# Kernel optimization log

Hardware: AMD Instinct MI355X
Metric: run time of the kernel (lower is better)

The kernel has to match this reference:

```python
import jax, jax.numpy as jnp
import numpy as np

EMB = 768
HEADS = 8
HEAD_DIM = EMB // HEADS  # 96
SCALING = HEAD_DIM ** -0.5


def setup_inputs() -> dict:
    key = jax.random.key(0)
    ks = jax.random.split(key, 9)
    B, S = 2, 2048
    std = 1.0 / np.sqrt(EMB)
    x = jax.random.normal(ks[0], (B, S, EMB), dtype=jnp.float32)
    # torch nn.Linear weights are [out, in]; we store [in, out] for x @ W.
    Wq = jax.random.normal(ks[1], (EMB, EMB), dtype=jnp.float32) * std
    Wk = jax.random.normal(ks[2], (EMB, EMB), dtype=jnp.float32) * std
    Wv = jax.random.normal(ks[3], (EMB, EMB), dtype=jnp.float32) * std
    Wo = jax.random.normal(ks[4], (EMB, EMB), dtype=jnp.float32) * std
    bq = jax.random.normal(ks[5], (EMB,), dtype=jnp.float32) * std
    bk = jax.random.normal(ks[6], (EMB,), dtype=jnp.float32) * std
    bv = jax.random.normal(ks[7], (EMB,), dtype=jnp.float32) * std
    bo = jax.random.normal(ks[8], (EMB,), dtype=jnp.float32) * std
    return {"x": x, "Wq": Wq, "bq": bq, "Wk": Wk, "bk": bk,
            "Wv": Wv, "bv": bv, "Wo": Wo, "bo": bo}


def _split_heads(t):
    # [B, S, E] -> [B, H, S, D]
    B, S, _ = t.shape
    return t.reshape(B, S, HEADS, HEAD_DIM).transpose(0, 2, 1, 3)


def reference(x, Wq, bq, Wk, bk, Wv, bv, Wo, bo):
    q = _split_heads(x @ Wq + bq)
    k = _split_heads(x @ Wk + bk)
    v = _split_heads(x @ Wv + bv)
    # Full [B, H, S, S] score matrix, as in the source module.
    energies = jnp.einsum('bhqd,bhkd->bhqk', q, k)
    # Faithful quirk: softmax first, THEN multiply by scaling (dropout=0 -> identity).
    attention = jax.nn.softmax(energies, axis=-1) * SCALING
    out = jnp.einsum('bhqk,bhkd->bhqd', attention, v)
    B, H, S, D = out.shape
    out = out.transpose(0, 2, 1, 3).reshape(B, S, H * D)
    return out @ Wo + bo
```

## Files before the change

kernel.cpp:

```cpp
#include <hip/hip_runtime.h>
#include <hip/hip_bf16.h>

#define EMB 768
#define HD 96
#define NH 8
#define SEQ 2048
#define SCALING 0.10206207261596575f

typedef short bf16x8 __attribute__((ext_vector_type(8)));
typedef float f32x4  __attribute__((ext_vector_type(4)));
typedef unsigned short u16v8 __attribute__((ext_vector_type(8)));
typedef unsigned short u16v4 __attribute__((ext_vector_type(4)));

union F4 { float4 v; float f[4]; };

__device__ __forceinline__ unsigned short f2bf(float v) {
    __hip_bfloat16 b = __float2bfloat16(v);
    return *reinterpret_cast<unsigned short*>(&b);
}
__device__ __forceinline__ float bf2f(unsigned short u) {
    __hip_bfloat16 b = *reinterpret_cast<__hip_bfloat16*>(&u);
    return __bfloat162float(b);
}

__device__ __forceinline__ void dma16(const unsigned short* g, unsigned short* l) {
    __builtin_amdgcn_global_load_lds(
        (const __attribute__((address_space(1))) unsigned int*)g,
        (__attribute__((address_space(3))) unsigned int*)l,
        16, 0, 0);
}

__global__ __launch_bounds__(256) void convert_x(
    const float* __restrict__ x,
    unsigned short* __restrict__ xh, unsigned short* __restrict__ xl)
{
    const size_t i0 = ((size_t)blockIdx.x * 256 + threadIdx.x) * 8;
    F4 a, b;
    a.v = *(const float4*)&x[i0];
    b.v = *(const float4*)&x[i0 + 4];
    u16v8 h, l;
    #pragma unroll
    for (int j = 0; j < 4; j++) {
        unsigned short hu = f2bf(a.f[j]);
        h[j] = hu; l[j] = f2bf(a.f[j] - bf2f(hu));
    }
    #pragma unroll
    for (int j = 0; j < 4; j++) {
        unsigned short hu = f2bf(b.f[j]);
        h[4+j] = hu; l[4+j] = f2bf(b.f[j] - bf2f(hu));
    }
    *(u16v8*)&xh[i0] = h;
    *(u16v8*)&xl[i0] = l;
}

__global__ __launch_bounds__(256) void convert_wT(
    const float* __restrict__ Wq, const float* __restrict__ Wk,
    const float* __restrict__ Wv, const float* __restrict__ Wo,
    unsigned short* __restrict__ WhT, unsigned short* __restrict__ WlT)
{
    const int z = blockIdx.z;
    const float* W = (z == 0) ? Wq : (z == 1) ? Wk : (z == 2) ? Wv : Wo;
    unsigned short* oh = WhT + (size_t)z * 589824;
    unsigned short* ol = WlT + (size_t)z * 589824;
    __shared__ float T[64][68];
    const int t = threadIdx.x;
    const int r = t >> 2, cg = (t & 3) * 16;
    const int k0 = blockIdx.x * 64, n0 = blockIdx.y * 64;
    #pragma unroll
    for (int i = 0; i < 4; i++) {
        float4 v = *(const float4*)&W[(size_t)(k0 + r) * EMB + n0 + cg + 4*i];
        *(float4*)&T[r][cg + 4*i] = v;
    }
    __syncthreads();
    #pragma unroll
    for (int i = 0; i < 4; i++) {
        u16v4 h, l;
        #pragma unroll
        for (int j = 0; j < 4; j++) {
            float v = T[cg + 4*i + j][r];
            unsigned short hu = f2bf(v);
            h[j] = hu; l[j] = f2bf(v - bf2f(hu));
        }
        *(u16v4*)&oh[(size_t)(n0 + r) * EMB + k0 + cg + 4*i] = h;
        *(u16v4*)&ol[(size_t)(n0 + r) * EMB + k0 + cg + 4*i] = l;
    }
}

#define QA_H 0
#define QA_L 4096
#define QW_H 8192
#define QW_L 12288

__global__ __launch_bounds__(256, 3) void qkv_mfma(
    const unsigned short* __restrict__ xh, const unsigned short* __restrict__ xl,
    const unsigned short* __restrict__ WhT, const unsigned short* __restrict__ WlT,
    const float* __restrict__ bq, const float* __restrict__ bk, const float* __restrict__ bv,
    unsigned short* __restrict__ Qh, unsigned short* __restrict__ Ql,
    unsigned short* __restrict__ Kb, unsigned short* __restrict__ Vt)
{
    const int which = blockIdx.z;
    const unsigned short* Wh = WhT + (size_t)which * 589824;
    const unsigned short* Wl = WlT + (size_t)which * 589824;
    const float* bias = (which == 0) ? bq : (which == 1) ? bk : bv;

    __shared__ __align__(16) unsigned short lds[16384];
    const int tid = threadIdx.x;
    const int lane = tid & 63, lo = lane & 15, h4 = lane >> 4;
    const int w = tid >> 6, wm = w & 1, wn = w >> 1;
    const int row0 = blockIdx.x * 128, col0 = blockIdx.y * 128;

    const unsigned short* sbase =
        (w == 0) ? xh + (size_t)row0 * EMB :
        (w == 1) ? xl + (size_t)row0 * EMB :
        (w == 2) ? Wh + (size_t)col0 * EMB :
                   Wl + (size_t)col0 * EMB;
    const int soff = w * 4096;

    f32x4 acc[4][4];
    #pragma unroll
    for (int i = 0; i < 4; i++)
        #pragma unroll
        for (int j = 0; j < 4; j++) acc[i][j] = (f32x4){0.f, 0.f, 0.f, 0.f};

    for (int k0 = 0; k0 < EMB; k0 += 32) {
        #pragma unroll
        for (int j = 0; j < 8; j++) {
            const int u = j*64 + lane;
            const int row = u >> 2, c8 = (u & 3) * 8;
            dma16(sbase + (size_t)row * EMB + k0 + c8, &lds[soff + j*512]);
        }
        __syncthreads();

        bf16x8 ah[4], al[4];
        #pragma unroll
        for (int i = 0; i < 4; i++)
            ah[i] = *(const bf16x8*)&lds[QA_H + (64*wm + 16*i + lo)*32 + 8*h4];
        if (which <= 1) {
            #pragma unroll
            for (int i = 0; i < 4; i++)
                al[i] = *(const bf16x8*)&lds[QA_L + (64*wm + 16*i + lo)*32 + 8*h4];
        }
        #pragma unroll
        for (int j = 0; j < 4; j++) {
            bf16x8 whf = *(const bf16x8*)&lds[QW_H + (64*wn + 16*j + lo)*32 + 8*h4];
            #pragma unroll
            for (int i = 0; i < 4; i++)
                acc[i][j] = __builtin_amdgcn_mfma_f32_16x16x32_bf16(ah[i], whf, acc[i][j], 0, 0, 0);
            if (which <= 1) {
                #pragma unroll
                for (int i = 0; i < 4; i++)
                    acc[i][j] = __builtin_amdgcn_mfma_f32_16x16x32_bf16(al[i], whf, acc[i][j], 0, 0, 0);
            }
            if (which != 1) {
                bf16x8 wlf = *(const bf16x8*)&lds[QW_L + (64*wn + 16*j + lo)*32 + 8*h4];
                #pragma unroll
                for (int i = 0; i < 4; i++)
                    acc[i][j] = __builtin_amdgcn_mfma_f32_16x16x32_bf16(ah[i], wlf, acc[i][j], 0, 0, 0);
            }
        }
        __syncthreads();
    }

    if (which == 0) {
        #pragma unroll
        for (int i = 0; i < 4; i++)
            #pragma unroll
            for (int r = 0; r < 4; r++) {
                const int sg = row0 + 64*wm + 16*i + 4*h4 + r;
                const int b = sg >> 11, s = sg & 2047;
                #pragma unroll
                for (int j = 0; j < 4; j++) {
                    const int c = col0 + 64*wn + 16*j + lo;
                    const int h = c / HD, d = c - h*HD;
                    float v = acc[i][j][r] + bias[c];
                    unsigned short hu = f2bf(v);
                    const size_t base = ((size_t)(b*NH + h) * SEQ + s) * HD + d;
                    Qh[base] = hu;
                    Ql[base] = f2bf(v - bf2f(hu));
                }
            }
    } else if (which == 1) {
        #pragma unroll
        for (int i = 0; i < 4; i++)
            #pragma unroll
            for (int r = 0; r < 4; r++) {
                const int sg = row0 + 64*wm + 16*i + 4*h4 + r;
                const int b = sg >> 11, s = sg & 2047;
                #pragma unroll
                for (int j = 0; j < 4; j++) {
                    const int c = col0 + 64*wn + 16*j + lo;
                    const int h = c / HD, d = c - h*HD;
                    float v = acc[i][j][r] + bias[c];
                    Kb[((size_t)(b*NH + h) * SEQ + s) * HD + d] = f2bf(v);
                }
            }
    } else {
        #pragma unroll
        for (int i = 0; i < 4; i++)
            #pragma unroll
            for (int r = 0; r < 4; r++) {
                const int sg = row0 + 64*wm + 16*i + 4*h4 + r;
                const int b = sg >> 11, s = sg & 2047;
                #pragma unroll
                for (int j = 0; j < 4; j++) {
                    const int c = col0 + 64*wn + 16*j + lo;
                    const int h = c / HD, d = c - h*HD;
                    float v = acc[i][j][r] + bias[c];
                    Vt[((size_t)(b*NH + h) * HD + d) * SEQ + s] = f2bf(v);
                }
            }
    }
}

#define PA_O 0
#define PWH_O 4096
#define PWL_O 6144

__global__ __launch_bounds__(256, 3) void proj_mfma(
    const unsigned short* __restrict__ AOh,
    const unsigned short* __restrict__ Wh, const unsigned short* __restrict__ Wl,
    const float* __restrict__ bo, float* __restrict__ out)
{
    __shared__ __align__(16) unsigned short lds[8192];
    const int tid = threadIdx.x;
    const int lane = tid & 63, lo = lane & 15, h4 = lane >> 4;
    const int w = tid >> 6, wm = w & 1, wn = w >> 1;
    const int row0 = blockIdx.x * 128, col0 = blockIdx.y * 64;

    const unsigned short* sbase =
        (w <= 1) ? AOh + (size_t)row0 * EMB :
        (w == 2) ? Wh  + (size_t)col0 * EMB :
                   Wl  + (size_t)col0 * EMB;
    const int jbase = (w == 1) ? 4 : 0;
    const int soff  = (w <= 1) ? PA_O : (w == 2) ? PWH_O : PWL_O;

    f32x4 acc[4][2];
    #pragma unroll
    for (int i = 0; i < 4; i++)
        #pragma unroll
        for (int j = 0; j < 2; j++) acc[i][j] = (f32x4){0.f, 0.f, 0.f, 0.f};

    for (int k0 = 0; k0 < EMB; k0 += 32) {
        #pragma unroll
        for (int jj = 0; jj < 4; jj++) {
            const int j = jbase + jj;
            const int u = j*64 + lane;
            const int row = u >> 2, c8 = (u & 3) * 8;
            dma16(sbase + (size_t)row * EMB + k0 + c8, &lds[soff + j*512]);
        }
        __syncthreads();

        bf16x8 af[4];
        #pragma unroll
        for (int i = 0; i < 4; i++)
            af[i] = *(const bf16x8*)&lds[PA_O + (64*wm + 16*i + lo)*32 + 8*h4];
        #pragma unroll
        for (int j = 0; j < 2; j++) {
            bf16x8 whf = *(const bf16x8*)&lds[PWH_O + (32*wn + 16*j + lo)*32 + 8*h4];
            bf16x8 wlf = *(const bf16x8*)&lds[PWL_O + (32*wn + 16*j + lo)*32 + 8*h4];
            #pragma unroll
            for (int i = 0; i < 4; i++) {
                acc[i][j] = __builtin_amdgcn_mfma_f32_16x16x32_bf16(af[i], whf, acc[i][j], 0, 0, 0);
                acc[i][j] = __builtin_amdgcn_mfma_f32_16x16x32_bf16(af[i], wlf, acc[i][j], 0, 0, 0);
            }
        }
        __syncthreads();
    }

    #pragma unroll
    for (int i = 0; i < 4; i++)
        #pragma unroll
        for (int r = 0; r < 4; r++) {
            const int sg = row0 + 64*wm + 16*i + 4*h4 + r;
            #pragma unroll
            for (int j = 0; j < 2; j++) {
                const int c = col0 + 32*wn + 16*j + lo;
                out[(size_t)sg * EMB + c] = acc[i][j][r] + bo[c];
            }
        }
}

#define AKB0 0
#define AVB0 6656
#define ABUF 13568
#define AP_OFF 27136

__global__ __launch_bounds__(256, 1) void attn_mfma(
    const unsigned short* __restrict__ Qh, const unsigned short* __restrict__ Ql,
    const unsigned short* __restrict__ Kb, const unsigned short* __restrict__ Vt,
    unsigned short* __restrict__ AOh)
{
    __shared__ __align__(16) unsigned short lds[36352];
    const int id   = blockIdx.x;
    const int xcd  = id & 7;
    const int j    = id >> 3;
    const int bh   = 2*xcd + (j & 1);
    const int q0   = (j >> 1) * 128;
    const int tid  = threadIdx.x;
    const int w    = tid >> 6;
    const int lane = tid & 63;
    const int lo   = lane & 15;
    const int h4   = lane >> 4;

    bf16x8 qhf[2][3], qlf[2][3];
    #pragma unroll
    for (int mi = 0; mi < 2; mi++) {
        const size_t qoff = ((size_t)bh*SEQ + q0 + 32*w + 16*mi + lo) * HD + 8*h4;
        #pragma unroll
        for (int ks = 0; ks < 3; ks++) {
            qhf[mi][ks] = *(const bf16x8*)&Qh[qoff + 32*ks];
            qlf[mi][ks] = *(const bf16x8*)&Ql[qoff + 32*ks];
        }
    }

    f32x4 O[2][6];
    #pragma unroll
    for (int mi = 0; mi < 2; mi++)
        #pragma unroll
        for (int i = 0; i < 6; i++) O[mi][i] = (f32x4){0.f, 0.f, 0.f, 0.f};
    float lsum[2][4] = {};

    unsigned short* Pw = lds + AP_OFF + w * 2304;
    const unsigned short* KbH = Kb + (size_t)bh * SEQ * HD;
    const unsigned short* VtH = Vt + (size_t)bh * HD * SEQ;

    #pragma unroll
    for (int r = 0; r < 3; r++) {
        const int u = tid + 256*r;
        const int kk = u / 12, g = u - kk*12;
        *(u16v8*)&lds[AKB0 + kk*104 + 8*g] = *(const u16v8*)&KbH[kk*HD + 8*g];
        const int dV = u >> 3, c8 = u & 7;
        *(u16v8*)&lds[AVB0 + dV*72 + 8*c8] = *(const u16v8*)&VtH[(size_t)dV*SEQ + 8*c8];
    }
    __syncthreads();

    #pragma unroll 1
    for (int c = 0; c < 32; c++) {
        unsigned short* curK = lds + (c & 1) * ABUF;
        unsigned short* curV = curK + 6656;
        unsigned short* nxtK = lds + ((c + 1) & 1) * ABUF;
        unsigned short* nxtV = nxtK + 6656;
        const int kn = (c + 1 < 32) ? (c + 1) * 64 : 0;

        u16v8 kst[3], vst[3];
        {
            const unsigned short* KG = KbH + (size_t)kn * HD;
            const unsigned short* VG = VtH + kn;
            #pragma unroll
            for (int r = 0; r < 3; r++) {
                const int u = tid + 256*r;
                const int kk = u / 12, g = u - kk*12;
                kst[r] = *(const u16v8*)&KG[kk*HD + 8*g];
                const int dV = u >> 3, c8 = u & 7;
                vst[r] = *(const u16v8*)&VG[(size_t)dV*SEQ + 8*c8];
            }
        }

        f32x4 S[2][4];
        #pragma unroll
        for (int mi = 0; mi < 2; mi++)
            #pragma unroll
            for (int nb = 0; nb < 4; nb++) S[mi][nb] = (f32x4){0.f, 0.f, 0.f, 0.f};
        #pragma unroll
        for (int ks = 0; ks < 3; ks++) {
            bf16x8 kf[4];
            #pragma unroll
            for (int nb = 0; nb < 4; nb++)
                kf[nb] = *(const bf16x8*)&curK[(16*nb + lo)*104 + 32*ks + 8*h4];
            #pragma unroll
            for (int nb = 0; nb < 4; nb++)
                #pragma unroll
                for (int mi = 0; mi < 2; mi++) {
                    S[mi][nb] = __builtin_amdgcn_mfma_f32_16x16x32_bf16(qhf[mi][ks], kf[nb], S[mi][nb], 0, 0, 0);
                    S[mi][nb] = __builtin_amdgcn_mfma_f32_16x16x32_bf16(qlf[mi][ks], kf[nb], S[mi][nb], 0, 0, 0);
                }
        }

        #pragma unroll
        for (int mi = 0; mi < 2; mi++)
            #pragma unroll
            for (int nb = 0; nb < 4; nb++)
                #pragma unroll
                for (int r = 0; r < 4; r++) {
                    float p = __expf(S[mi][nb][r]);
                    lsum[mi][r] += p;
                    Pw[(16*mi + 4*h4 + r)*72 + 16*nb + lo] = f2bf(p);
                }

        #pragma unroll
        for (int ks2 = 0; ks2 < 2; ks2++) {
            bf16x8 pf0 = *(const bf16x8*)&Pw[(lo)*72      + 32*ks2 + 8*h4];
            bf16x8 pf1 = *(const bf16x8*)&Pw[(16 + lo)*72 + 32*ks2 + 8*h4];
            #pragma unroll
            for (int nb2 = 0; nb2 < 6; nb2++) {
                bf16x8 vfv = *(const bf16x8*)&curV[(16*nb2 + lo)*72 + 32*ks2 + 8*h4];
                O[0][nb2] = __builtin_amdgcn_mfma_f32_16x16x32_bf16(pf0, vfv, O[0][nb2], 0, 0, 0);
                O[1][nb2] = __builtin_amdgcn_mfma_f32_16x16x32_bf16(pf1, vfv, O[1][nb2], 0, 0, 0);
            }
        }

        #pragma unroll
        for (int r = 0; r < 3; r++) {
            const int u = tid + 256*r;
            const int kk = u / 12, g = u - kk*12;
            *(u16v8*)&nxtK[kk*104 + 8*g] = kst[r];
            const int dV = u >> 3, c8 = u & 7;
            *(u16v8*)&nxtV[dV*72 + 8*c8] = vst[r];
        }
        __syncthreads();
    }

    const int b = bh >> 3, hh = bh & 7;
    #pragma unroll
    for (int mi = 0; mi < 2; mi++)
        #pragma unroll
        for (int r = 0; r < 4; r++) {
            float l = lsum[mi][r];
            l += __shfl_xor(l, 1);
            l += __shfl_xor(l, 2);
            l += __shfl_xor(l, 4);
            l += __shfl_xor(l, 8);
            const float sc = SCALING / l;
            const int q = q0 + 32*w + 16*mi + 4*h4 + r;
            const size_t base = ((size_t)b*SEQ + q)*EMB + hh*HD + lo;
            #pragma unroll
            for (int nb2 = 0; nb2 < 6; nb2++)
                AOh[base + 16*nb2] = f2bf(O[mi][nb2][r] * sc);
        }
}

extern "C" void kernel_launch(void* const* d_in, const int* in_sizes, int n_in,
                              void* d_out, int out_size, void* d_ws, size_t ws_size,
                              hipStream_t stream)
{
    const float* x  = (const float*)d_in[0];
    const float* Wq = (const float*)d_in[1];
    const float* bq = (const float*)d_in[2];
    const float* Wk = (const float*)d_in[3];
    const float* bk = (const float*)d_in[4];
    const float* Wv = (const float*)d_in[5];
    const float* bv = (const float*)d_in[6];
    const float* Wo = (const float*)d_in[7];
    const float* bo = (const float*)d_in[8];
    float* out = (float*)d_out;

    unsigned short* ws = (unsigned short*)d_ws;
    const size_t HS = (size_t)16 * SEQ * HD;
    const size_t WS1 = (size_t)EMB * EMB;
    unsigned short* Qh  = ws;
    unsigned short* Ql  = ws + HS;
    unsigned short* Kb  = ws + 2*HS;
    unsigned short* Vt  = ws + 3*HS;
    unsigned short* xh  = ws + 4*HS;
    unsigned short* xl  = ws + 5*HS;
    unsigned short* WhT = ws + 6*HS;
    unsigned short* WlT = ws + 6*HS + 4*WS1;
    unsigned short* AOh = xh;

    convert_x<<<1536, 256, 0, stream>>>(x, xh, xl);
    convert_wT<<<dim3(12, 12, 4), 256, 0, stream>>>(Wq, Wk, Wv, Wo, WhT, WlT);
    qkv_mfma<<<dim3(32, 6, 3), 256, 0, stream>>>(xh, xl, WhT, WlT, bq, bk, bv,
                                                 Qh, Ql, Kb, Vt);
    attn_mfma<<<256, 256, 0, stream>>>(Qh, Ql, Kb, Vt, AOh);
    proj_mfma<<<dim3(32, 12), 256, 0, stream>>>(AOh, WhT + 3*WS1, WlT + 3*WS1, bo, out);
}
```

Before: 215.8 us.

## Split attention block into 8 waves of 16 query rows each

The attention kernel now runs 512 threads per block, with each wave owning 16 query rows instead of 32. Per-wave register state (Q fragments, O accumulators, S tiles) is halved, and the K/V tile staging is spread over more threads, so each thread issues one load per round instead of two. The aim is more waves per CU to hide latency. In exchange, each K/V fragment read from LDS now feeds only one query tile, which doubles LDS read traffic per unit of MFMA work, and block-wide barriers now cover 8 waves.

Result: faster. 207.7 us (-3.8%).

```diff
diff --git a/kernel.cpp b/kernel.cpp
--- a/kernel.cpp
+++ b/kernel.cpp
@@ -285,7 +285,7 @@
 #define ABUF 13568
 #define AP_OFF 27136
 
-__global__ __launch_bounds__(256, 1) void attn_mfma(
+__global__ __launch_bounds__(512, 2) void attn_mfma(
     const unsigned short* __restrict__ Qh, const unsigned short* __restrict__ Ql,
     const unsigned short* __restrict__ Kb, const unsigned short* __restrict__ Vt,
     unsigned short* __restrict__ AOh)
@@ -302,35 +302,36 @@
     const int lo   = lane & 15;
     const int h4   = lane >> 4;
 
-    bf16x8 qhf[2][3], qlf[2][3];
-    #pragma unroll
-    for (int mi = 0; mi < 2; mi++) {
-        const size_t qoff = ((size_t)bh*SEQ + q0 + 32*w + 16*mi + lo) * HD + 8*h4;
+    bf16x8 qhf[3], qlf[3];
+    {
+        const size_t qoff = ((size_t)bh*SEQ + q0 + 16*w + lo) * HD + 8*h4;
         #pragma unroll
         for (int ks = 0; ks < 3; ks++) {
-            qhf[mi][ks] = *(const bf16x8*)&Qh[qoff + 32*ks];
-            qlf[mi][ks] = *(const bf16x8*)&Ql[qoff + 32*ks];
-        }
-    }
-
-    f32x4 O[2][6];
-    #pragma unroll
-    for (int mi = 0; mi < 2; mi++)
-        #pragma unroll
-        for (int i = 0; i < 6; i++) O[mi][i] = (f32x4){0.f, 0.f, 0.f, 0.f};
-    float lsum[2][4] = {};
-
-    unsigned short* Pw = lds + AP_OFF + w * 2304;
+            qhf[ks] = *(const bf16x8*)&Qh[qoff + 32*ks];
+            qlf[ks] = *(const bf16x8*)&Ql[qoff + 32*ks];
+        }
+    }
+
+    f32x4 O[6];
+    #pragma unroll
+    for (int i = 0; i < 6; i++) O[i] = (f32x4){0.f, 0.f, 0.f, 0.f};
+    float lsum[4] = {};
+
+    unsigned short* Pw = lds + AP_OFF + w * 1152;
     const unsigned short* KbH = Kb + (size_t)bh * SEQ * HD;
     const unsigned short* VtH = Vt + (size_t)bh * HD * SEQ;
 
     #pragma unroll
     for (int r = 0; r < 3; r++) {
-        const int u = tid + 256*r;
-        const int kk = u / 12, g = u - kk*12;
-        *(u16v8*)&lds[AKB0 + kk*104 + 8*g] = *(const u16v8*)&KbH[kk*HD + 8*g];
-        const int dV = u >> 3, c8 = u & 7;
-        *(u16v8*)&lds[AVB0 + dV*72 + 8*c8] = *(const u16v8*)&VtH[(size_t)dV*SEQ + 8*c8];
+        const int u = tid + 512*r;
+        if (u < 768) {
+            const int kk = u / 12, g = u - kk*12;
+            *(u16v8*)&lds[AKB0 + kk*104 + 8*g] = *(const u16v8*)&KbH[kk*HD + 8*g];
+        } else {
+            const int uv = u - 768;
+            const int dV = uv >> 3, c8 = uv & 7;
+            *(u16v8*)&lds[AVB0 + dV*72 + 8*c8] = *(const u16v8*)&VtH[(size_t)dV*SEQ + 8*c8];
+        }
     }
     __syncthreads();
 
@@ -342,25 +343,27 @@
         unsigned short* nxtV = nxtK + 6656;
         const int kn = (c + 1 < 32) ? (c + 1) * 64 : 0;
 
-        u16v8 kst[3], vst[3];
+        u16v8 st[3];
         {
             const unsigned short* KG = KbH + (size_t)kn * HD;
             const unsigned short* VG = VtH + kn;
             #pragma unroll
             for (int r = 0; r < 3; r++) {
-                const int u = tid + 256*r;
-                const int kk = u / 12, g = u - kk*12;
-                kst[r] = *(const u16v8*)&KG[kk*HD + 8*g];
-                const int dV = u >> 3, c8 = u & 7;
-                vst[r] = *(const u16v8*)&VG[(size_t)dV*SEQ + 8*c8];
-            }
-        }
-
-        f32x4 S[2][4];
-        #pragma unroll
-        for (int mi = 0; mi < 2; mi++)
-            #pragma unroll
-            for (int nb = 0; nb < 4; nb++) S[mi][nb] = (f32x4){0.f, 0.f, 0.f, 0.f};
+                const int u = tid + 512*r;
+                if (u < 768) {
+                    const int kk = u / 12, g = u - kk*12;
+                    st[r] = *(const u16v8*)&KG[kk*HD + 8*g];
+                } else {
+                    const int uv = u - 768;
+                    const int dV = uv >> 3, c8 = uv & 7;
+                    st[r] = *(const u16v8*)&VG[(size_t)dV*SEQ + 8*c8];
+                }
+            }
+        }
+
+        f32x4 S[4];
+        #pragma unroll
+        for (int nb = 0; nb < 4; nb++) S[nb] = (f32x4){0.f, 0.f, 0.f, 0.f};
         #pragma unroll
         for (int ks = 0; ks < 3; ks++) {
             bf16x8 kf[4];
@@ -368,65 +371,61 @@
             for (int nb = 0; nb < 4; nb++)
                 kf[nb] = *(const bf16x8*)&curK[(16*nb + lo)*104 + 32*ks + 8*h4];
             #pragma unroll
-            for (int nb = 0; nb < 4; nb++)
-                #pragma unroll
-                for (int mi = 0; mi < 2; mi++) {
-                    S[mi][nb] = __builtin_amdgcn_mfma_f32_16x16x32_bf16(qhf[mi][ks], kf[nb], S[mi][nb], 0, 0, 0);
-                    S[mi][nb] = __builtin_amdgcn_mfma_f32_16x16x32_bf16(qlf[mi][ks], kf[nb], S[mi][nb], 0, 0, 0);
-                }
-        }
-
-        #pragma unroll
-        for (int mi = 0; mi < 2; mi++)
-            #pragma unroll
-            for (int nb = 0; nb < 4; nb++)
-                #pragma unroll
-                for (int r = 0; r < 4; r++) {
-                    float p = __expf(S[mi][nb][r]);
-                    lsum[mi][r] += p;
-                    Pw[(16*mi + 4*h4 + r)*72 + 16*nb + lo] = f2bf(p);
-                }
+            for (int nb = 0; nb < 4; nb++) {
+                S[nb] = __builtin_amdgcn_mfma_f32_16x16x32_bf16(qhf[ks], kf[nb], S[nb], 0, 0, 0);
+                S[nb] = __builtin_amdgcn_mfma_f32_16x16x32_bf16(qlf[ks], kf[nb], S[nb], 0, 0, 0);
+            }
+        }
+
+        #pragma unroll
+        for (int nb = 0; nb < 4; nb++)
+            #pragma unroll
+            for (int r = 0; r < 4; r++) {
+                float p = __expf(S[nb][r]);
+                lsum[r] += p;
+                Pw[(4*h4 + r)*72 + 16*nb + lo] = f2bf(p);
+            }
 
         #pragma unroll
         for (int ks2 = 0; ks2 < 2; ks2++) {
-            bf16x8 pf0 = *(const bf16x8*)&Pw[(lo)*72      + 32*ks2 + 8*h4];
-            bf16x8 pf1 = *(const bf16x8*)&Pw[(16 + lo)*72 + 32*ks2 + 8*h4];
+            bf16x8 pf = *(const bf16x8*)&Pw[lo*72 + 32*ks2 + 8*h4];
             #pragma unroll
             for (int nb2 = 0; nb2 < 6; nb2++) {
                 bf16x8 vfv = *(const bf16x8*)&curV[(16*nb2 + lo)*72 + 32*ks2 + 8*h4];
-                O[0][nb2] = __builtin_amdgcn_mfma_f32_16x16x32_bf16(pf0, vfv, O[0][nb2], 0, 0, 0);
-                O[1][nb2] = __builtin_amdgcn_mfma_f32_16x16x32_bf16(pf1, vfv, O[1][nb2], 0, 0, 0);
+                O[nb2] = __builtin_amdgcn_mfma_f32_16x16x32_bf16(pf, vfv, O[nb2], 0, 0, 0);
             }
         }
 
         #pragma unroll
         for (int r = 0; r < 3; r++) {
-            const int u = tid + 256*r;
-            const int kk = u / 12, g = u - kk*12;
-            *(u16v8*)&nxtK[kk*104 + 8*g] = kst[r];
-            const int dV = u >> 3, c8 = u & 7;
-            *(u16v8*)&nxtV[dV*72 + 8*c8] = vst[r];
+            const int u = tid + 512*r;
+            if (u < 768) {
+                const int kk = u / 12, g = u - kk*12;
+                *(u16v8*)&nxtK[kk*104 + 8*g] = st[r];
+            } else {
+                const int uv = u - 768;
+                const int dV = uv >> 3, c8 = uv & 7;
+                *(u16v8*)&nxtV[dV*72 + 8*c8] = st[r];
+            }
         }
         __syncthreads();
     }
 
     const int b = bh >> 3, hh = bh & 7;
     #pragma unroll
-    for (int mi = 0; mi < 2; mi++)
-        #pragma unroll
-        for (int r = 0; r < 4; r++) {
-            float l = lsum[mi][r];
-            l += __shfl_xor(l, 1);
-            l += __shfl_xor(l, 2);
-            l += __shfl_xor(l, 4);
-            l += __shfl_xor(l, 8);
-            const float sc = SCALING / l;
-            const int q = q0 + 32*w + 16*mi + 4*h4 + r;
-            const size_t base = ((size_t)b*SEQ + q)*EMB + hh*HD + lo;
-            #pragma unroll
-            for (int nb2 = 0; nb2 < 6; nb2++)
-                AOh[base + 16*nb2] = f2bf(O[mi][nb2][r] * sc);
-        }
+    for (int r = 0; r < 4; r++) {
+        float l = lsum[r];
+        l += __shfl_xor(l, 1);
+        l += __shfl_xor(l, 2);
+        l += __shfl_xor(l, 4);
+        l += __shfl_xor(l, 8);
+        const float sc = SCALING / l;
+        const int q = q0 + 16*w + 4*h4 + r;
+        const size_t base = ((size_t)b*SEQ + q)*EMB + hh*HD + lo;
+        #pragma unroll
+        for (int nb2 = 0; nb2 < 6; nb2++)
+            AOh[base + 16*nb2] = f2bf(O[nb2][r] * sc);
+    }
 }
 
 extern "C" void kernel_launch(void* const* d_in, const int* in_sizes, int n_in,
@@ -461,6 +460,6 @@
     convert_wT<<<dim3(12, 12, 4), 256, 0, stream>>>(Wq, Wk, Wv, Wo, WhT, WlT);
     qkv_mfma<<<dim3(32, 6, 3), 256, 0, stream>>>(xh, xl, WhT, WlT, bq, bk, bv,
                                                  Qh, Ql, Kb, Vt);
-    attn_mfma<<<256, 256, 0, stream>>>(Qh, Ql, Kb, Vt, AOh);
+    attn_mfma<<<256, 512, 0, stream>>>(Qh, Ql, Kb, Vt, AOh);
     proj_mfma<<<dim3(32, 12), 256, 0, stream>>>(AOh, WhT + 3*WS1, WlT + 3*WS1, bo, out);
 }
```

## Split attention KV sequence across two wave groups per block and merge partials

Applied to the files above, without the earlier changes.

The attention kernel now uses 512 threads per block. Two groups of four waves each process alternate 64-key chunks of the same 128-query tile, and both chunks of a pair are loaded into LDS per iteration. The second group writes its partial O and row sums to LDS at the end, and the first group combines them and writes the output. This doubles the waves per CU to hide MFMA and memory latency and halves the serial loop length. In exchange it doubles LDS use and adds a final reduction pass with an extra barrier.

Result: faster. 206.0 us (-4.6%).

```diff
diff --git a/kernel.cpp b/kernel.cpp
--- a/kernel.cpp
+++ b/kernel.cpp
@@ -280,17 +280,16 @@
         }
 }
 
-#define AKB0 0
-#define AVB0 6656
-#define ABUF 13568
-#define AP_OFF 27136
-
-__global__ __launch_bounds__(256, 1) void attn_mfma(
+#define ACH 13568
+#define APAIR 27136
+#define AP_OFF 54272
+
+__global__ __launch_bounds__(512, 2) void attn_mfma(
     const unsigned short* __restrict__ Qh, const unsigned short* __restrict__ Ql,
     const unsigned short* __restrict__ Kb, const unsigned short* __restrict__ Vt,
     unsigned short* __restrict__ AOh)
 {
-    __shared__ __align__(16) unsigned short lds[36352];
+    __shared__ __align__(16) unsigned short lds[72704];
     const int id   = blockIdx.x;
     const int xcd  = id & 7;
     const int j    = id >> 3;
@@ -298,14 +297,40 @@
     const int q0   = (j >> 1) * 128;
     const int tid  = threadIdx.x;
     const int w    = tid >> 6;
+    const int g    = w >> 2;
+    const int wq   = w & 3;
     const int lane = tid & 63;
     const int lo   = lane & 15;
     const int h4   = lane >> 4;
 
+    const unsigned short* KbH = Kb + (size_t)bh * SEQ * HD;
+    const unsigned short* VtH = Vt + (size_t)bh * HD * SEQ;
+
+    const unsigned short* sp0[6];
+    int fK[6];
+    int doff[6];
+    #pragma unroll
+    for (int r = 0; r < 6; r++) {
+        const int e  = tid + 512*r;
+        const int ch = (e >= 1536) ? 1 : 0;
+        const int e2 = e - ch*1536;
+        if (e2 < 768) {
+            const int kk = e2 / 12, g8 = e2 - kk*12;
+            sp0[r]  = KbH + (size_t)(ch*64 + kk) * HD + 8*g8;
+            fK[r]   = HD;
+            doff[r] = ch*ACH + kk*104 + 8*g8;
+        } else {
+            const int uv = e2 - 768, dV = uv >> 3, c8 = uv & 7;
+            sp0[r]  = VtH + (size_t)dV*SEQ + ch*64 + 8*c8;
+            fK[r]   = 1;
+            doff[r] = ch*ACH + 6656 + dV*72 + 8*c8;
+        }
+    }
+
     bf16x8 qhf[2][3], qlf[2][3];
     #pragma unroll
     for (int mi = 0; mi < 2; mi++) {
-        const size_t qoff = ((size_t)bh*SEQ + q0 + 32*w + 16*mi + lo) * HD + 8*h4;
+        const size_t qoff = ((size_t)bh*SEQ + q0 + 32*wq + 16*mi + lo) * HD + 8*h4;
         #pragma unroll
         for (int ks = 0; ks < 3; ks++) {
             qhf[mi][ks] = *(const bf16x8*)&Qh[qoff + 32*ks];
@@ -321,40 +346,22 @@
     float lsum[2][4] = {};
 
     unsigned short* Pw = lds + AP_OFF + w * 2304;
-    const unsigned short* KbH = Kb + (size_t)bh * SEQ * HD;
-    const unsigned short* VtH = Vt + (size_t)bh * HD * SEQ;
-
-    #pragma unroll
-    for (int r = 0; r < 3; r++) {
-        const int u = tid + 256*r;
-        const int kk = u / 12, g = u - kk*12;
-        *(u16v8*)&lds[AKB0 + kk*104 + 8*g] = *(const u16v8*)&KbH[kk*HD + 8*g];
-        const int dV = u >> 3, c8 = u & 7;
-        *(u16v8*)&lds[AVB0 + dV*72 + 8*c8] = *(const u16v8*)&VtH[(size_t)dV*SEQ + 8*c8];
-    }
+
+    #pragma unroll
+    for (int r = 0; r < 6; r++)
+        *(u16v8*)&lds[doff[r]] = *(const u16v8*)sp0[r];
     __syncthreads();
 
     #pragma unroll 1
-    for (int c = 0; c < 32; c++) {
-        unsigned short* curK = lds + (c & 1) * ABUF;
-        unsigned short* curV = curK + 6656;
-        unsigned short* nxtK = lds + ((c + 1) & 1) * ABUF;
-        unsigned short* nxtV = nxtK + 6656;
-        const int kn = (c + 1 < 32) ? (c + 1) * 64 : 0;
-
-        u16v8 kst[3], vst[3];
-        {
-            const unsigned short* KG = KbH + (size_t)kn * HD;
-            const unsigned short* VG = VtH + kn;
-            #pragma unroll
-            for (int r = 0; r < 3; r++) {
-                const int u = tid + 256*r;
-                const int kk = u / 12, g = u - kk*12;
-                kst[r] = *(const u16v8*)&KG[kk*HD + 8*g];
-                const int dV = u >> 3, c8 = u & 7;
-                vst[r] = *(const u16v8*)&VG[(size_t)dV*SEQ + 8*c8];
-            }
-        }
+    for (int u = 0; u < 16; u++) {
+        const int kn0 = (u < 15) ? 128*(u + 1) : 0;
+        u16v8 st[6];
+        #pragma unroll
+        for (int r = 0; r < 6; r++)
+            st[r] = *(const u16v8*)(sp0[r] + (size_t)kn0 * fK[r]);
+
+        const unsigned short* myK = lds + (u & 1)*APAIR + g*ACH;
+        const unsigned short* myV = myK + 6656;
 
         f32x4 S[2][4];
         #pragma unroll
@@ -366,7 +373,7 @@
             bf16x8 kf[4];
             #pragma unroll
             for (int nb = 0; nb < 4; nb++)
-                kf[nb] = *(const bf16x8*)&curK[(16*nb + lo)*104 + 32*ks + 8*h4];
+                kf[nb] = *(const bf16x8*)&myK[(16*nb + lo)*104 + 32*ks + 8*h4];
             #pragma unroll
             for (int nb = 0; nb < 4; nb++)
                 #pragma unroll
@@ -393,40 +400,54 @@
             bf16x8 pf1 = *(const bf16x8*)&Pw[(16 + lo)*72 + 32*ks2 + 8*h4];
             #pragma unroll
             for (int nb2 = 0; nb2 < 6; nb2++) {
-                bf16x8 vfv = *(const bf16x8*)&curV[(16*nb2 + lo)*72 + 32*ks2 + 8*h4];
+                bf16x8 vfv = *(const bf16x8*)&myV[(16*nb2 + lo)*72 + 32*ks2 + 8*h4];
                 O[0][nb2] = __builtin_amdgcn_mfma_f32_16x16x32_bf16(pf0, vfv, O[0][nb2], 0, 0, 0);
                 O[1][nb2] = __builtin_amdgcn_mfma_f32_16x16x32_bf16(pf1, vfv, O[1][nb2], 0, 0, 0);
             }
         }
 
-        #pragma unroll
-        for (int r = 0; r < 3; r++) {
-            const int u = tid + 256*r;
-            const int kk = u / 12, g = u - kk*12;
-            *(u16v8*)&nxtK[kk*104 + 8*g] = kst[r];
-            const int dV = u >> 3, c8 = u & 7;
-            *(u16v8*)&nxtV[dV*72 + 8*c8] = vst[r];
-        }
+        unsigned short* dstp = lds + ((u + 1) & 1)*APAIR;
+        #pragma unroll
+        for (int r = 0; r < 6; r++)
+            *(u16v8*)&dstp[doff[r]] = st[r];
         __syncthreads();
     }
 
-    const int b = bh >> 3, hh = bh & 7;
-    #pragma unroll
-    for (int mi = 0; mi < 2; mi++)
-        #pragma unroll
-        for (int r = 0; r < 4; r++) {
-            float l = lsum[mi][r];
-            l += __shfl_xor(l, 1);
-            l += __shfl_xor(l, 2);
-            l += __shfl_xor(l, 4);
-            l += __shfl_xor(l, 8);
-            const float sc = SCALING / l;
-            const int q = q0 + 32*w + 16*mi + 4*h4 + r;
-            const size_t base = ((size_t)b*SEQ + q)*EMB + hh*HD + lo;
-            #pragma unroll
-            for (int nb2 = 0; nb2 < 6; nb2++)
-                AOh[base + 16*nb2] = f2bf(O[mi][nb2][r] * sc);
-        }
+    float* Fo = (float*)lds;
+    float* Ls = (float*)lds + 12288;
+    if (g == 1) {
+        #pragma unroll
+        for (int mi = 0; mi < 2; mi++)
+            #pragma unroll
+            for (int r = 0; r < 4; r++) {
+                const int ql = 32*wq + 16*mi + 4*h4 + r;
+                Ls[ql*16 + lo] = lsum[mi][r];
+                #pragma unroll
+                for (int nb2 = 0; nb2 < 6; nb2++)
+                    Fo[ql*96 + 16*nb2 + lo] = O[mi][nb2][r];
+            }
+    }
+    __syncthreads();
+    if (g == 0) {
+        const int b = bh >> 3, hh = bh & 7;
+        #pragma unroll
+        for (int mi = 0; mi < 2; mi++)
+            #pragma unroll
+            for (int r = 0; r < 4; r++) {
+                const int ql = 32*wq + 16*mi + 4*h4 + r;
+                float l = lsum[mi][r] + Ls[ql*16 + lo];
+                l += __shfl_xor(l, 1);
+                l += __shfl_xor(l, 2);
+                l += __shfl_xor(l, 4);
+                l += __shfl_xor(l, 8);
+                const float sc = SCALING / l;
+                const int q = q0 + ql;
+                const size_t base = ((size_t)b*SEQ + q)*EMB + hh*HD + lo;
+                #pragma unroll
+                for (int nb2 = 0; nb2 < 6; nb2++)
+                    AOh[base + 16*nb2] = f2bf((O[mi][nb2][r] + Fo[ql*96 + 16*nb2 + lo]) * sc);
+            }
+    }
 }
 
 extern "C" void kernel_launch(void* const* d_in, const int* in_sizes, int n_in,
@@ -461,6 +482,6 @@
     convert_wT<<<dim3(12, 12, 4), 256, 0, stream>>>(Wq, Wk, Wv, Wo, WhT, WlT);
     qkv_mfma<<<dim3(32, 6, 3), 256, 0, stream>>>(xh, xl, WhT, WlT, bq, bk, bv,
                                                  Qh, Ql, Kb, Vt);
-    attn_mfma<<<256, 256, 0, stream>>>(Qh, Ql, Kb, Vt, AOh);
+    attn_mfma<<<256, 512, 0, stream>>>(Qh, Ql, Kb, Vt, AOh);
     proj_mfma<<<dim3(32, 12), 256, 0, stream>>>(AOh, WhT + 3*WS1, WlT + 3*WS1, bo, out);
 }
```
